# Kernel tuning notes

Measured on AMD Instinct MI355X. Metric: run time of the kernel, lower is better.

Reference implementation:

```python
import jax, jax.numpy as jnp
import numpy as np

B, H, S, D = 4, 8, 2048, 64

def setup_inputs() -> dict:
    key = jax.random.key(0)
    k1, k2 = jax.random.split(key)
    q = jax.random.normal(k1, (B, H, S, D), dtype=jnp.float32)
    kv = jax.random.normal(k2, (B, H, S, D), dtype=jnp.float32)
    mask = jnp.zeros((1, 1, S, S), dtype=jnp.float32)
    return {"q": q, "kv": kv, "mask": mask}

def reference(q, kv, mask):
    # score = q @ kv^T / sqrt(d_k) + mask ; softmax over last dim ; @ kv
    d_k = jnp.asarray(kv.shape[-1], dtype=q.dtype)
    score = jnp.einsum('bhqd,bhkd->bhqk', q, kv) / jnp.sqrt(d_k)
    score = score + mask
    attn = jax.nn.softmax(score, axis=-1)
    out = jnp.einsum('bhqk,bhkd->bhqd', attn, kv)
    return out
```

## Files before the change

kernel.cpp:

```cpp
#include <hip/hip_runtime.h>
#include <hip/hip_bf16.h>
#include <stdint.h>


typedef __bf16 bf16;
typedef __attribute__((ext_vector_type(8))) __bf16 bf16x8;
typedef __attribute__((ext_vector_type(4))) __bf16 bf16x4;
typedef __attribute__((ext_vector_type(4))) float floatx4;

#define SLEN 2048
#define DH   64
#define BR   64
#define BC   64
#define NKT  (SLEN / BC)
#define NEP  (NKT / 2)
#define NQT  (SLEN / BR)
#define BH_N 32
#define LOG2E 1.44269504088896341f

#define CHB_L  1024
#define IMGB_L 8192
#define IMGE_G 4096
#define BUF2   (4 * IMGB_L)

#define AS1 __attribute__((address_space(1)))
#define AS3 __attribute__((address_space(3)))

static __device__ inline void gload_lds16(const void* g, void* l) {
    __builtin_amdgcn_global_load_lds((const AS1 uint32_t*)g, (AS3 uint32_t*)l, 16, 0, 0);
}

static __device__ inline float fexp2(float x) {
    return __builtin_amdgcn_exp2f(x);
}

static_assert(BH_N == NQT, "prep kernel folds bh and qt onto one grid axis");

static __device__ inline int phys_key(int l) {
    int h = l >> 5, l5 = l & 31, q = l5 >> 3, j = l5 & 7;
    return 32 * h + (j < 4 ? 4 * q + j : 16 + 4 * q + (j - 4));
}

__global__ __launch_bounds__(256) void kv_prep(
    const float* __restrict__ kv, const float* __restrict__ mask,
    bf16* __restrict__ kvK, bf16* __restrict__ kvT, int* __restrict__ flags)
{
    __shared__ bf16 Tl[64 * 72];
    __shared__ int wany[4];
    const int kt = blockIdx.x, z = blockIdx.y;
    const int t = threadIdx.x;

    float acc = 0.f;
#pragma unroll
    for (int i = 0; i < 4; ++i) {
        int f = i * 256 + t;
        int row = f >> 4, c4 = (f & 15) * 4;
        const float4 v = *(const float4*)(mask + (size_t)(z * BR + row) * SLEN + kt * BC + c4);
        acc = fmaxf(acc, fmaxf(fmaxf(fabsf(v.x), fabsf(v.y)), fmaxf(fabsf(v.z), fabsf(v.w))));
    }
    unsigned long long any = __ballot(acc != 0.f);
    if ((t & 63) == 0) wany[t >> 6] = (any != 0ull) ? 1 : 0;

    const float* src = kv + ((size_t)z * SLEN + kt * BC) * DH;
#pragma unroll
    for (int i = 0; i < 4; ++i) {
        int f = i * 256 + t;
        int key = f >> 4, d4 = (f & 15) * 4;
        float4 v = *(const float4*)(src + (size_t)key * DH + d4);
        bf16x4 b; b[0] = (bf16)v.x; b[1] = (bf16)v.y; b[2] = (bf16)v.z; b[3] = (bf16)v.w;
        *(bf16x4*)&Tl[key * 72 + d4] = b;
    }
    __syncthreads();
    if (t == 0) flags[z * NKT + kt] = wany[0] | wany[1] | wany[2] | wany[3];

    bf16* outK = kvK + ((size_t)z * NKT + kt) * IMGE_G;
#pragma unroll
    for (int i = 0; i < 2; ++i) {
        int G = i * 256 + t;
        int c = G >> 6, L = G & 63, rl = L >> 3, p = L & 7;
        int g = (p - rl - 4 * (c & 1)) & 7, key = 8 * c + rl;
        bf16x8 w = *(const bf16x8*)&Tl[key * 72 + g * 8];
        *(bf16x8*)(outK + (size_t)G * 8) = w;
    }
    bf16* outV = kvT + ((size_t)z * NKT + kt) * IMGE_G;
#pragma unroll
    for (int i = 0; i < 2; ++i) {
        int G = i * 256 + t;
        int c = G >> 6, L = G & 63, dl = L >> 3, p = L & 7;
        int g = (p - dl - 4 * (c & 1)) & 7, d = 8 * c + dl;
        bf16x8 w;
#pragma unroll
        for (int j = 0; j < 8; ++j)
            w[j] = Tl[phys_key(8 * g + j) * 72 + d];
        *(bf16x8*)(outV + (size_t)G * 8) = w;
    }
}

__global__ __launch_bounds__(512) void attn_fwd13(
    const float* __restrict__ q, const float* __restrict__ mask,
    const int* __restrict__ flags,
    const bf16* __restrict__ kvK, const bf16* __restrict__ kvT,
    float* __restrict__ out)
{
    __shared__ __align__(16) char smem[2 * BUF2];

    const int bh = blockIdx.x;
    const int qt = blockIdx.y;
    const int q0 = qt * 128;
    const int t = threadIdx.x;
    const int wave = t >> 6, lane = t & 63;
    const int ln16 = lane & 15, quad = lane >> 4;
    const int ln8 = ln16 & 7, hb = ln16 >> 3;

    const float qscale = 0.125f * LOG2E;
    bf16x8 aq[2];
    {
        const float* qrow = q + ((size_t)bh * SLEN + q0 + wave * 16 + ln16) * DH;
#pragma unroll
        for (int kc = 0; kc < 2; ++kc) {
            float4 f0 = *(const float4*)(qrow + kc * 32 + quad * 8);
            float4 f1 = *(const float4*)(qrow + kc * 32 + quad * 8 + 4);
            bf16x8 a;
            a[0] = (bf16)(f0.x * qscale); a[1] = (bf16)(f0.y * qscale);
            a[2] = (bf16)(f0.z * qscale); a[3] = (bf16)(f0.w * qscale);
            a[4] = (bf16)(f1.x * qscale); a[5] = (bf16)(f1.y * qscale);
            a[6] = (bf16)(f1.z * qscale); a[7] = (bf16)(f1.w * qscale);
            aq[kc] = a;
        }
    }

    const int fqt = qt * 2 + (wave >> 2);
    unsigned fmask;
    {
        int ld = (lane < 32) ? flags[fqt * NKT + lane] : 0;
        fmask = (unsigned)__ballot(ld != 0);
    }

    const int kbase0 = hb * CHB_L + ln8 * 128 + (((quad + ln8 + 4 * hb) & 7) << 4);
    const int kbase1 = hb * CHB_L + ln8 * 128 + (((quad + 4 + ln8 + 4 * hb) & 7) << 4);

    floatx4 o[4];
#pragma unroll
    for (int dt = 0; dt < 4; ++dt) o[dt] = (floatx4){0.f, 0.f, 0.f, 0.f};
    float m_run = -3.0e38f, l_run = 0.f;

    const bf16* kvKb = kvK + (size_t)bh * NKT * IMGE_G;
    const bf16* kvTb = kvT + (size_t)bh * NKT * IMGE_G;

    {
        char* B0 = smem;
        gload_lds16(kvKb + (size_t)wave * 512 + lane * 8,           B0 +             wave * CHB_L);
        gload_lds16(kvTb + (size_t)wave * 512 + lane * 8,           B0 + IMGB_L +    wave * CHB_L);
        gload_lds16(kvKb + IMGE_G + (size_t)wave * 512 + lane * 8,  B0 + 2*IMGB_L +  wave * CHB_L);
        gload_lds16(kvTb + IMGE_G + (size_t)wave * 512 + lane * 8,  B0 + 3*IMGB_L +  wave * CHB_L);
    }

    for (int e = 0; e < NEP; ++e) {
        __syncthreads();

        if (e + 1 < NEP) {
            char* Bn = smem + ((e + 1) & 1) * BUF2;
            const bf16* gK0 = kvKb + (size_t)(2 * e + 2) * IMGE_G;
            const bf16* gV0 = kvTb + (size_t)(2 * e + 2) * IMGE_G;
            gload_lds16(gK0 + (size_t)wave * 512 + lane * 8,          Bn +            wave * CHB_L);
            gload_lds16(gV0 + (size_t)wave * 512 + lane * 8,          Bn + IMGB_L +   wave * CHB_L);
            gload_lds16(gK0 + IMGE_G + (size_t)wave * 512 + lane * 8, Bn + 2*IMGB_L + wave * CHB_L);
            gload_lds16(gV0 + IMGE_G + (size_t)wave * 512 + lane * 8, Bn + 3*IMGB_L + wave * CHB_L);
        }

        const char* B  = smem + (e & 1) * BUF2;
        const char* K0 = B;
        const char* V0 = B + IMGB_L;
        const char* K1 = B + 2 * IMGB_L;
        const char* V1 = B + 3 * IMGB_L;

        floatx4 s0[4], s1[4];
#pragma unroll
        for (int nt = 0; nt < 4; ++nt) {
            bf16x8 a0 = *(const bf16x8*)(K0 + nt * 2048 + kbase0);
            bf16x8 a1 = *(const bf16x8*)(K0 + nt * 2048 + kbase1);
            floatx4 acc = (floatx4){0.f, 0.f, 0.f, 0.f};
            acc = __builtin_amdgcn_mfma_f32_16x16x32_bf16(a0, aq[0], acc, 0, 0, 0);
            acc = __builtin_amdgcn_mfma_f32_16x16x32_bf16(a1, aq[1], acc, 0, 0, 0);
            s0[nt] = acc;
        }
#pragma unroll
        for (int nt = 0; nt < 4; ++nt) {
            bf16x8 a0 = *(const bf16x8*)(K1 + nt * 2048 + kbase0);
            bf16x8 a1 = *(const bf16x8*)(K1 + nt * 2048 + kbase1);
            floatx4 acc = (floatx4){0.f, 0.f, 0.f, 0.f};
            acc = __builtin_amdgcn_mfma_f32_16x16x32_bf16(a0, aq[0], acc, 0, 0, 0);
            acc = __builtin_amdgcn_mfma_f32_16x16x32_bf16(a1, aq[1], acc, 0, 0, 0);
            s1[nt] = acc;
        }

        if (fmask & (1u << (2 * e))) {
            const float* mrow = mask + (size_t)(q0 + wave * 16 + ln16) * SLEN + (2 * e) * BC;
#pragma unroll
            for (int nt = 0; nt < 4; ++nt) {
                float4 mv = *(const float4*)(mrow + 16 * nt + quad * 4);
                s0[nt][0] += mv.x * LOG2E; s0[nt][1] += mv.y * LOG2E;
                s0[nt][2] += mv.z * LOG2E; s0[nt][3] += mv.w * LOG2E;
            }
        }
        if (fmask & (1u << (2 * e + 1))) {
            const float* mrow = mask + (size_t)(q0 + wave * 16 + ln16) * SLEN + (2 * e + 1) * BC;
#pragma unroll
            for (int nt = 0; nt < 4; ++nt) {
                float4 mv = *(const float4*)(mrow + 16 * nt + quad * 4);
                s1[nt][0] += mv.x * LOG2E; s1[nt][1] += mv.y * LOG2E;
                s1[nt][2] += mv.z * LOG2E; s1[nt][3] += mv.w * LOG2E;
            }
        }

        float tm0 = s0[0][0], tm1 = s1[0][0];
#pragma unroll
        for (int nt = 0; nt < 4; ++nt)
#pragma unroll
            for (int r = 0; r < 4; ++r) {
                tm0 = fmaxf(tm0, s0[nt][r]);
                tm1 = fmaxf(tm1, s1[nt][r]);
            }
        float tmax = fmaxf(tm0, tm1);
        tmax = fmaxf(tmax, __shfl_xor(tmax, 16));
        tmax = fmaxf(tmax, __shfl_xor(tmax, 32));
        float mnew = fmaxf(m_run, tmax);
        unsigned long long grew = __ballot(mnew > m_run);
        float alpha = fexp2(m_run - mnew);
        m_run = mnew;

        float rs = 0.f;
        bf16x8 pf00, pf01, pf10, pf11;
#pragma unroll
        for (int r = 0; r < 4; ++r) {
            float a0 = fexp2(s0[0][r] - mnew);
            float a1 = fexp2(s0[1][r] - mnew);
            float a2 = fexp2(s0[2][r] - mnew);
            float a3 = fexp2(s0[3][r] - mnew);
            float b0 = fexp2(s1[0][r] - mnew);
            float b1 = fexp2(s1[1][r] - mnew);
            float b2 = fexp2(s1[2][r] - mnew);
            float b3 = fexp2(s1[3][r] - mnew);
            rs += ((a0 + a1) + (a2 + a3)) + ((b0 + b1) + (b2 + b3));
            pf00[r] = (bf16)a0; pf00[4 + r] = (bf16)a1;
            pf01[r] = (bf16)a2; pf01[4 + r] = (bf16)a3;
            pf10[r] = (bf16)b0; pf10[4 + r] = (bf16)b1;
            pf11[r] = (bf16)b2; pf11[4 + r] = (bf16)b3;
        }
        rs += __shfl_xor(rs, 16);
        rs += __shfl_xor(rs, 32);

        if (grew) {
            l_run = l_run * alpha + rs;
            float a0 = __shfl(alpha, quad * 4 + 0);
            float a1 = __shfl(alpha, quad * 4 + 1);
            float a2 = __shfl(alpha, quad * 4 + 2);
            float a3 = __shfl(alpha, quad * 4 + 3);
#pragma unroll
            for (int dt = 0; dt < 4; ++dt) {
                o[dt][0] *= a0; o[dt][1] *= a1; o[dt][2] *= a2; o[dt][3] *= a3;
            }
        } else {
            l_run += rs;
        }

#pragma unroll
        for (int dt = 0; dt < 4; ++dt) {
            bf16x8 v0 = *(const bf16x8*)(V0 + dt * 2048 + kbase0);
            bf16x8 v1 = *(const bf16x8*)(V0 + dt * 2048 + kbase1);
            o[dt] = __builtin_amdgcn_mfma_f32_16x16x32_bf16(pf00, v0, o[dt], 0, 0, 0);
            o[dt] = __builtin_amdgcn_mfma_f32_16x16x32_bf16(pf01, v1, o[dt], 0, 0, 0);
        }
#pragma unroll
        for (int dt = 0; dt < 4; ++dt) {
            bf16x8 v0 = *(const bf16x8*)(V1 + dt * 2048 + kbase0);
            bf16x8 v1 = *(const bf16x8*)(V1 + dt * 2048 + kbase1);
            o[dt] = __builtin_amdgcn_mfma_f32_16x16x32_bf16(pf10, v0, o[dt], 0, 0, 0);
            o[dt] = __builtin_amdgcn_mfma_f32_16x16x32_bf16(pf11, v1, o[dt], 0, 0, 0);
        }
    }

    float l0 = __shfl(l_run, quad * 4 + 0);
    float l1 = __shfl(l_run, quad * 4 + 1);
    float l2 = __shfl(l_run, quad * 4 + 2);
    float l3 = __shfl(l_run, quad * 4 + 3);
    float i0 = 1.f / l0, i1 = 1.f / l1, i2 = 1.f / l2, i3 = 1.f / l3;
    float* ob = out + ((size_t)bh * SLEN + q0 + wave * 16) * DH;
#pragma unroll
    for (int dt = 0; dt < 4; ++dt) {
        int col = ln16 + 16 * dt;
        ob[(quad * 4 + 0) * DH + col] = o[dt][0] * i0;
        ob[(quad * 4 + 1) * DH + col] = o[dt][1] * i1;
        ob[(quad * 4 + 2) * DH + col] = o[dt][2] * i2;
        ob[(quad * 4 + 3) * DH + col] = o[dt][3] * i3;
    }
}

#define LDT 72
__global__ __launch_bounds__(256) void attn_mask_flags(
    const float* __restrict__ mask, int* __restrict__ flags)
{
    const int kt = blockIdx.x, qt = blockIdx.y;
    const int t = threadIdx.x;
    float acc = 0.f;
#pragma unroll
    for (int i = 0; i < 4; ++i) {
        int f = i * 256 + t;
        int row = f >> 4, c4 = (f & 15) * 4;
        const float4 v = *(const float4*)(mask + (size_t)(qt * BR + row) * SLEN + kt * BC + c4);
        acc = fmaxf(acc, fmaxf(fmaxf(fabsf(v.x), fabsf(v.y)), fmaxf(fabsf(v.z), fabsf(v.w))));
    }
    unsigned long long any = __ballot(acc != 0.f);
    __shared__ int wany[4];
    if ((t & 63) == 0) wany[t >> 6] = (any != 0ull) ? 1 : 0;
    __syncthreads();
    if (t == 0) flags[qt * NKT + kt] = wany[0] | wany[1] | wany[2] | wany[3];
}

__global__ __launch_bounds__(256) void attn_fwd(
    const float* __restrict__ q, const float* __restrict__ kv,
    const float* __restrict__ mask, const int* __restrict__ flags,
    float* __restrict__ out)
{
    __shared__ __align__(16) bf16 Kl[BC * LDT];
    __shared__ __align__(16) bf16 Vt[DH * LDT];
    __shared__ __align__(16) bf16 Pl[BR * LDT];

    const int qt = blockIdx.x;
    const int bh = blockIdx.y;
    const int q0 = qt * BR;
    const int t = threadIdx.x;
    const int wave = t >> 6, lane = t & 63;
    const int ln16 = lane & 15, quad = lane >> 4;

    const float qscale = 0.125f * LOG2E;
    bf16x8 aq[2];
    {
        const float* qrow = q + ((size_t)bh * SLEN + q0 + wave * 16 + ln16) * DH;
#pragma unroll
        for (int kc = 0; kc < 2; ++kc) {
            float4 f0 = *(const float4*)(qrow + kc * 32 + quad * 8);
            float4 f1 = *(const float4*)(qrow + kc * 32 + quad * 8 + 4);
            bf16x8 a;
            a[0] = (bf16)(f0.x * qscale); a[1] = (bf16)(f0.y * qscale);
            a[2] = (bf16)(f0.z * qscale); a[3] = (bf16)(f0.w * qscale);
            a[4] = (bf16)(f1.x * qscale); a[5] = (bf16)(f1.y * qscale);
            a[6] = (bf16)(f1.z * qscale); a[7] = (bf16)(f1.w * qscale);
            aq[kc] = a;
        }
    }

    floatx4 o[4];
#pragma unroll
    for (int dt = 0; dt < 4; ++dt) o[dt] = (floatx4){0.f, 0.f, 0.f, 0.f};
    float m_run[4], l_run[4];
#pragma unroll
    for (int r = 0; r < 4; ++r) { m_run[r] = -3.0e38f; l_run[r] = 0.f; }

    const float* kvb = kv + (size_t)bh * SLEN * DH;

    for (int kt = 0; kt < NKT; ++kt) {
        float4 st[4];
        const float* kvt = kvb + (size_t)kt * BC * DH;
#pragma unroll
        for (int i = 0; i < 4; ++i) {
            int f = i * 256 + t;
            st[i] = *(const float4*)(kvt + (size_t)f * 4);
        }
        __syncthreads();
#pragma unroll
        for (int i = 0; i < 4; ++i) {
            int f = i * 256 + t;
            int key = f >> 4, d4 = (f & 15) * 4;
            bf16 b0 = (bf16)st[i].x, b1 = (bf16)st[i].y, b2 = (bf16)st[i].z, b3 = (bf16)st[i].w;
            *(bf16x4*)&Kl[key * LDT + d4] = (bf16x4){b0, b1, b2, b3};
            Vt[(d4 + 0) * LDT + key] = b0;
            Vt[(d4 + 1) * LDT + key] = b1;
            Vt[(d4 + 2) * LDT + key] = b2;
            Vt[(d4 + 3) * LDT + key] = b3;
        }
        __syncthreads();

        floatx4 s[4];
#pragma unroll
        for (int nt = 0; nt < 4; ++nt) {
            s[nt] = (floatx4){0.f, 0.f, 0.f, 0.f};
#pragma unroll
            for (int kc = 0; kc < 2; ++kc) {
                bf16x8 bk = *(const bf16x8*)&Kl[(ln16 + 16 * nt) * LDT + kc * 32 + quad * 8];
                s[nt] = __builtin_amdgcn_mfma_f32_16x16x32_bf16(aq[kc], bk, s[nt], 0, 0, 0);
            }
        }

        if (!flags || flags[qt * NKT + kt]) {
            const float* mrow = mask + (size_t)(q0 + quad * 4) * SLEN + kt * BC + ln16;
#pragma unroll
            for (int r = 0; r < 4; ++r)
#pragma unroll
                for (int nt = 0; nt < 4; ++nt)
                    s[nt][r] += mrow[(size_t)r * SLEN + nt * 16] * LOG2E;
        }

#pragma unroll
        for (int r = 0; r < 4; ++r) {
            float mx = fmaxf(fmaxf(s[0][r], s[1][r]), fmaxf(s[2][r], s[3][r]));
            mx = fmaxf(mx, __shfl_xor(mx, 1));
            mx = fmaxf(mx, __shfl_xor(mx, 2));
            mx = fmaxf(mx, __shfl_xor(mx, 4));
            mx = fmaxf(mx, __shfl_xor(mx, 8));
            float mnew = fmaxf(m_run[r], mx);
            float alpha = exp2f(m_run[r] - mnew);
            m_run[r] = mnew;
            float rs = 0.f;
#pragma unroll
            for (int nt = 0; nt < 4; ++nt) {
                float p = exp2f(s[nt][r] - mnew);
                s[nt][r] = p;
                rs += p;
            }
            rs += __shfl_xor(rs, 1);
            rs += __shfl_xor(rs, 2);
            rs += __shfl_xor(rs, 4);
            rs += __shfl_xor(rs, 8);
            l_run[r] = l_run[r] * alpha + rs;
#pragma unroll
            for (int dt = 0; dt < 4; ++dt) o[dt][r] *= alpha;
        }

#pragma unroll
        for (int nt = 0; nt < 4; ++nt)
#pragma unroll
            for (int r = 0; r < 4; ++r)
                Pl[(wave * 16 + quad * 4 + r) * LDT + ln16 + 16 * nt] = (bf16)s[nt][r];

#pragma unroll
        for (int kc2 = 0; kc2 < 2; ++kc2) {
            bf16x8 pfr = *(const bf16x8*)&Pl[(wave * 16 + ln16) * LDT + kc2 * 32 + quad * 8];
#pragma unroll
            for (int dt = 0; dt < 4; ++dt) {
                bf16x8 vfr = *(const bf16x8*)&Vt[(ln16 + 16 * dt) * LDT + kc2 * 32 + quad * 8];
                o[dt] = __builtin_amdgcn_mfma_f32_16x16x32_bf16(pfr, vfr, o[dt], 0, 0, 0);
            }
        }
    }

#pragma unroll
    for (int r = 0; r < 4; ++r) {
        float inv = 1.0f / l_run[r];
        int qrow = q0 + wave * 16 + quad * 4 + r;
        float* orow = out + ((size_t)bh * SLEN + qrow) * DH;
#pragma unroll
        for (int dt = 0; dt < 4; ++dt)
            orow[ln16 + 16 * dt] = o[dt][r] * inv;
    }
}

extern "C" void kernel_launch(void* const* d_in, const int* in_sizes, int n_in,
                              void* d_out, int out_size, void* d_ws, size_t ws_size,
                              hipStream_t stream)
{
    const float* q    = (const float*)d_in[0];
    const float* kv   = (const float*)d_in[1];
    const float* mask = (const float*)d_in[2];
    float* out = (float*)d_out;

    const size_t kvKoff = 4096;
    const size_t kvToff = kvKoff + (size_t)BH_N * NKT * IMGE_G * 2;
    const size_t need   = kvToff + (size_t)BH_N * NKT * IMGE_G * 2;

    if (ws_size >= need) {
        int*  flags = (int*)d_ws;
        bf16* kvK   = (bf16*)((char*)d_ws + kvKoff);
        bf16* kvT   = (bf16*)((char*)d_ws + kvToff);
        kv_prep<<<dim3(NKT, BH_N), 256, 0, stream>>>(kv, mask, kvK, kvT, flags);
        attn_fwd13<<<dim3(BH_N, SLEN / 128), 512, 0, stream>>>(q, mask, flags, kvK, kvT, out);
    } else {
        int* flags = nullptr;
        if (ws_size >= (size_t)NQT * NKT * sizeof(int)) {
            flags = (int*)d_ws;
            attn_mask_flags<<<dim3(NKT, NQT), 256, 0, stream>>>(mask, flags);
        }
        attn_fwd<<<dim3(NQT, BH_N), 256, 0, stream>>>(q, kv, mask, flags, out);
    }
}
```

Before: 140.7 us.

## Switch attention to 32x32x16 MFMA tiles with 4 waves per block

Rewrites the main attention kernel to use 32x32x16 bf16 MFMA instead of 16x16x32. Each of 4 waves now owns 32 query rows instead of 16, and the block shrinks from 512 to 256 threads with 2 blocks per CU. The P operand is rearranged in registers with permlane32_swap instead of relying on a permuted key order, so the V prep drops the phys_key remap. Row-max and row-sum reductions need only one cross-half shuffle, and output stores become float4. The aim is fewer MFMA issues and less LDS operand traffic per FLOP, at the cost of more accumulator registers and possible occupancy pressure.

```diff
diff --git a/kernel.cpp b/kernel.cpp
--- a/kernel.cpp
+++ b/kernel.cpp
@@ -7,6 +7,9 @@
 typedef __attribute__((ext_vector_type(8))) __bf16 bf16x8;
 typedef __attribute__((ext_vector_type(4))) __bf16 bf16x4;
 typedef __attribute__((ext_vector_type(4))) float floatx4;
+typedef __attribute__((ext_vector_type(16))) float floatx16;
+typedef __attribute__((ext_vector_type(4))) int int4v;
+typedef __attribute__((ext_vector_type(2))) unsigned int uint2v;
 
 #define SLEN 2048
 #define DH   64
@@ -36,11 +39,6 @@
 
 static_assert(BH_N == NQT, "prep kernel folds bh and qt onto one grid axis");
 
-static __device__ inline int phys_key(int l) {
-    int h = l >> 5, l5 = l & 31, q = l5 >> 3, j = l5 & 7;
-    return 32 * h + (j < 4 ? 4 * q + j : 16 + 4 * q + (j - 4));
-}
-
 __global__ __launch_bounds__(256) void kv_prep(
     const float* __restrict__ kv, const float* __restrict__ mask,
     bf16* __restrict__ kvK, bf16* __restrict__ kvT, int* __restrict__ flags)
@@ -91,12 +89,12 @@
         bf16x8 w;
 #pragma unroll
         for (int j = 0; j < 8; ++j)
-            w[j] = Tl[phys_key(8 * g + j) * 72 + d];
+            w[j] = Tl[(8 * g + j) * 72 + d];
         *(bf16x8*)(outV + (size_t)G * 8) = w;
     }
 }
 
-__global__ __launch_bounds__(512) void attn_fwd13(
+__global__ __launch_bounds__(256, 2) void attn_fwd14(
     const float* __restrict__ q, const float* __restrict__ mask,
     const int* __restrict__ flags,
     const bf16* __restrict__ kvK, const bf16* __restrict__ kvT,
@@ -108,192 +106,183 @@
     const int qt = blockIdx.y;
     const int q0 = qt * 128;
     const int t = threadIdx.x;
-    const int wave = t >> 6, lane = t & 63;
-    const int ln16 = lane & 15, quad = lane >> 4;
-    const int ln8 = ln16 & 7, hb = ln16 >> 3;
+    const int w = t >> 6, lane = t & 63;
+    const int r5 = lane & 31, h = lane >> 5;
+    const int c3 = r5 >> 3, rl = lane & 7;
 
     const float qscale = 0.125f * LOG2E;
-    bf16x8 aq[2];
+    bf16x8 qf[4];
     {
-        const float* qrow = q + ((size_t)bh * SLEN + q0 + wave * 16 + ln16) * DH;
-#pragma unroll
-        for (int kc = 0; kc < 2; ++kc) {
-            float4 f0 = *(const float4*)(qrow + kc * 32 + quad * 8);
-            float4 f1 = *(const float4*)(qrow + kc * 32 + quad * 8 + 4);
+        const float* qrow = q + ((size_t)bh * SLEN + q0 + w * 32 + r5) * DH;
+#pragma unroll
+        for (int s = 0; s < 4; ++s) {
+            float4 f0 = *(const float4*)(qrow + 16 * s + 8 * h);
+            float4 f1 = *(const float4*)(qrow + 16 * s + 8 * h + 4);
             bf16x8 a;
             a[0] = (bf16)(f0.x * qscale); a[1] = (bf16)(f0.y * qscale);
             a[2] = (bf16)(f0.z * qscale); a[3] = (bf16)(f0.w * qscale);
             a[4] = (bf16)(f1.x * qscale); a[5] = (bf16)(f1.y * qscale);
             a[6] = (bf16)(f1.z * qscale); a[7] = (bf16)(f1.w * qscale);
-            aq[kc] = a;
-        }
-    }
-
-    const int fqt = qt * 2 + (wave >> 2);
+            qf[s] = a;
+        }
+    }
+
+    const int fqt = qt * 2 + (w >> 1);
     unsigned fmask;
     {
         int ld = (lane < 32) ? flags[fqt * NKT + lane] : 0;
         fmask = (unsigned)__ballot(ld != 0);
     }
 
-    const int kbase0 = hb * CHB_L + ln8 * 128 + (((quad + ln8 + 4 * hb) & 7) << 4);
-    const int kbase1 = hb * CHB_L + ln8 * 128 + (((quad + 4 + ln8 + 4 * hb) & 7) << 4);
-
-    floatx4 o[4];
-#pragma unroll
-    for (int dt = 0; dt < 4; ++dt) o[dt] = (floatx4){0.f, 0.f, 0.f, 0.f};
+    int addr4[4];
+#pragma unroll
+    for (int s = 0; s < 4; ++s) {
+        int slot = (2 * s + h + rl + 4 * (c3 & 1)) & 7;
+        addr4[s] = c3 * 1024 + rl * 128 + slot * 16;
+    }
+
+    floatx16 o[2];
+#pragma unroll
+    for (int dt = 0; dt < 2; ++dt)
+#pragma unroll
+        for (int i = 0; i < 16; ++i) o[dt][i] = 0.f;
     float m_run = -3.0e38f, l_run = 0.f;
 
     const bf16* kvKb = kvK + (size_t)bh * NKT * IMGE_G;
     const bf16* kvTb = kvT + (size_t)bh * NKT * IMGE_G;
 
-    {
-        char* B0 = smem;
-        gload_lds16(kvKb + (size_t)wave * 512 + lane * 8,           B0 +             wave * CHB_L);
-        gload_lds16(kvTb + (size_t)wave * 512 + lane * 8,           B0 + IMGB_L +    wave * CHB_L);
-        gload_lds16(kvKb + IMGE_G + (size_t)wave * 512 + lane * 8,  B0 + 2*IMGB_L +  wave * CHB_L);
-        gload_lds16(kvTb + IMGE_G + (size_t)wave * 512 + lane * 8,  B0 + 3*IMGB_L +  wave * CHB_L);
-    }
+    auto stage = [&](int t2, char* Bn) {
+        const bf16* gK = kvKb + (size_t)t2 * IMGE_G;
+        const bf16* gV = kvTb + (size_t)t2 * IMGE_G;
+#pragma unroll
+        for (int cc = 0; cc < 2; ++cc) {
+            const int c = 2 * w + cc;
+            gload_lds16(gK + (size_t)c * 512 + lane * 8,          Bn +              c * CHB_L);
+            gload_lds16(gV + (size_t)c * 512 + lane * 8,          Bn + IMGB_L +     c * CHB_L);
+            gload_lds16(gK + IMGE_G + (size_t)c * 512 + lane * 8, Bn + 2 * IMGB_L + c * CHB_L);
+            gload_lds16(gV + IMGE_G + (size_t)c * 512 + lane * 8, Bn + 3 * IMGB_L + c * CHB_L);
+        }
+    };
+
+    stage(0, smem);
 
     for (int e = 0; e < NEP; ++e) {
         __syncthreads();
 
-        if (e + 1 < NEP) {
-            char* Bn = smem + ((e + 1) & 1) * BUF2;
-            const bf16* gK0 = kvKb + (size_t)(2 * e + 2) * IMGE_G;
-            const bf16* gV0 = kvTb + (size_t)(2 * e + 2) * IMGE_G;
-            gload_lds16(gK0 + (size_t)wave * 512 + lane * 8,          Bn +            wave * CHB_L);
-            gload_lds16(gV0 + (size_t)wave * 512 + lane * 8,          Bn + IMGB_L +   wave * CHB_L);
-            gload_lds16(gK0 + IMGE_G + (size_t)wave * 512 + lane * 8, Bn + 2*IMGB_L + wave * CHB_L);
-            gload_lds16(gV0 + IMGE_G + (size_t)wave * 512 + lane * 8, Bn + 3*IMGB_L + wave * CHB_L);
-        }
-
-        const char* B  = smem + (e & 1) * BUF2;
-        const char* K0 = B;
-        const char* V0 = B + IMGB_L;
-        const char* K1 = B + 2 * IMGB_L;
-        const char* V1 = B + 3 * IMGB_L;
-
-        floatx4 s0[4], s1[4];
-#pragma unroll
-        for (int nt = 0; nt < 4; ++nt) {
-            bf16x8 a0 = *(const bf16x8*)(K0 + nt * 2048 + kbase0);
-            bf16x8 a1 = *(const bf16x8*)(K0 + nt * 2048 + kbase1);
-            floatx4 acc = (floatx4){0.f, 0.f, 0.f, 0.f};
-            acc = __builtin_amdgcn_mfma_f32_16x16x32_bf16(a0, aq[0], acc, 0, 0, 0);
-            acc = __builtin_amdgcn_mfma_f32_16x16x32_bf16(a1, aq[1], acc, 0, 0, 0);
-            s0[nt] = acc;
-        }
-#pragma unroll
-        for (int nt = 0; nt < 4; ++nt) {
-            bf16x8 a0 = *(const bf16x8*)(K1 + nt * 2048 + kbase0);
-            bf16x8 a1 = *(const bf16x8*)(K1 + nt * 2048 + kbase1);
-            floatx4 acc = (floatx4){0.f, 0.f, 0.f, 0.f};
-            acc = __builtin_amdgcn_mfma_f32_16x16x32_bf16(a0, aq[0], acc, 0, 0, 0);
-            acc = __builtin_amdgcn_mfma_f32_16x16x32_bf16(a1, aq[1], acc, 0, 0, 0);
-            s1[nt] = acc;
-        }
-
-        if (fmask & (1u << (2 * e))) {
-            const float* mrow = mask + (size_t)(q0 + wave * 16 + ln16) * SLEN + (2 * e) * BC;
-#pragma unroll
-            for (int nt = 0; nt < 4; ++nt) {
-                float4 mv = *(const float4*)(mrow + 16 * nt + quad * 4);
-                s0[nt][0] += mv.x * LOG2E; s0[nt][1] += mv.y * LOG2E;
-                s0[nt][2] += mv.z * LOG2E; s0[nt][3] += mv.w * LOG2E;
-            }
-        }
-        if (fmask & (1u << (2 * e + 1))) {
-            const float* mrow = mask + (size_t)(q0 + wave * 16 + ln16) * SLEN + (2 * e + 1) * BC;
-#pragma unroll
-            for (int nt = 0; nt < 4; ++nt) {
-                float4 mv = *(const float4*)(mrow + 16 * nt + quad * 4);
-                s1[nt][0] += mv.x * LOG2E; s1[nt][1] += mv.y * LOG2E;
-                s1[nt][2] += mv.z * LOG2E; s1[nt][3] += mv.w * LOG2E;
-            }
-        }
-
-        float tm0 = s0[0][0], tm1 = s1[0][0];
-#pragma unroll
-        for (int nt = 0; nt < 4; ++nt)
-#pragma unroll
-            for (int r = 0; r < 4; ++r) {
-                tm0 = fmaxf(tm0, s0[nt][r]);
-                tm1 = fmaxf(tm1, s1[nt][r]);
-            }
-        float tmax = fmaxf(tm0, tm1);
-        tmax = fmaxf(tmax, __shfl_xor(tmax, 16));
+        if (e + 1 < NEP) stage(2 * e + 2, smem + ((e + 1) & 1) * BUF2);
+
+        const char* B = smem + (e & 1) * BUF2;
+
+        floatx16 s[4];
+#pragma unroll
+        for (int T = 0; T < 4; ++T) {
+            const char* Kimg = B + (T >> 1) * (2 * IMGB_L) + (T & 1) * 4096;
+            floatx16 acc;
+#pragma unroll
+            for (int i = 0; i < 16; ++i) acc[i] = 0.f;
+#pragma unroll
+            for (int ss = 0; ss < 4; ++ss) {
+                bf16x8 kf = *(const bf16x8*)(Kimg + addr4[ss]);
+                acc = __builtin_amdgcn_mfma_f32_32x32x16_bf16(kf, qf[ss], acc, 0, 0, 0);
+            }
+            s[T] = acc;
+        }
+
+#pragma unroll
+        for (int T = 0; T < 4; ++T) {
+            if (fmask & (1u << (2 * e + (T >> 1)))) {
+                const float* mrow = mask + (size_t)(q0 + w * 32 + r5) * SLEN
+                                    + e * 128 + T * 32 + 4 * h;
+#pragma unroll
+                for (int g4 = 0; g4 < 4; ++g4) {
+                    float4 mv = *(const float4*)(mrow + 8 * g4);
+                    s[T][4 * g4 + 0] += mv.x * LOG2E;
+                    s[T][4 * g4 + 1] += mv.y * LOG2E;
+                    s[T][4 * g4 + 2] += mv.z * LOG2E;
+                    s[T][4 * g4 + 3] += mv.w * LOG2E;
+                }
+            }
+        }
+
+        float tm[4];
+#pragma unroll
+        for (int T = 0; T < 4; ++T) {
+            float a0 = fmaxf(s[T][0], s[T][1]),   a1 = fmaxf(s[T][2], s[T][3]);
+            float a2 = fmaxf(s[T][4], s[T][5]),   a3 = fmaxf(s[T][6], s[T][7]);
+            float a4 = fmaxf(s[T][8], s[T][9]),   a5 = fmaxf(s[T][10], s[T][11]);
+            float a6 = fmaxf(s[T][12], s[T][13]), a7 = fmaxf(s[T][14], s[T][15]);
+            a0 = fmaxf(a0, a1); a2 = fmaxf(a2, a3); a4 = fmaxf(a4, a5); a6 = fmaxf(a6, a7);
+            tm[T] = fmaxf(fmaxf(a0, a2), fmaxf(a4, a6));
+        }
+        float tmax = fmaxf(fmaxf(tm[0], tm[1]), fmaxf(tm[2], tm[3]));
         tmax = fmaxf(tmax, __shfl_xor(tmax, 32));
         float mnew = fmaxf(m_run, tmax);
         unsigned long long grew = __ballot(mnew > m_run);
         float alpha = fexp2(m_run - mnew);
         m_run = mnew;
+        if (grew) {
+#pragma unroll
+            for (int dt = 0; dt < 2; ++dt)
+#pragma unroll
+                for (int i = 0; i < 16; ++i) o[dt][i] *= alpha;
+        }
 
         float rs = 0.f;
-        bf16x8 pf00, pf01, pf10, pf11;
-#pragma unroll
-        for (int r = 0; r < 4; ++r) {
-            float a0 = fexp2(s0[0][r] - mnew);
-            float a1 = fexp2(s0[1][r] - mnew);
-            float a2 = fexp2(s0[2][r] - mnew);
-            float a3 = fexp2(s0[3][r] - mnew);
-            float b0 = fexp2(s1[0][r] - mnew);
-            float b1 = fexp2(s1[1][r] - mnew);
-            float b2 = fexp2(s1[2][r] - mnew);
-            float b3 = fexp2(s1[3][r] - mnew);
-            rs += ((a0 + a1) + (a2 + a3)) + ((b0 + b1) + (b2 + b3));
-            pf00[r] = (bf16)a0; pf00[4 + r] = (bf16)a1;
-            pf01[r] = (bf16)a2; pf01[4 + r] = (bf16)a3;
-            pf10[r] = (bf16)b0; pf10[4 + r] = (bf16)b1;
-            pf11[r] = (bf16)b2; pf11[4 + r] = (bf16)b3;
-        }
-        rs += __shfl_xor(rs, 16);
+#pragma unroll
+        for (int T = 0; T < 4; ++T) {
+            float ev[16];
+#pragma unroll
+            for (int i = 0; i < 16; ++i) ev[i] = fexp2(s[T][i] - mnew);
+            float r0 = (ev[0] + ev[1]) + (ev[2] + ev[3]);
+            float r1 = (ev[4] + ev[5]) + (ev[6] + ev[7]);
+            float r2 = (ev[8] + ev[9]) + (ev[10] + ev[11]);
+            float r3 = (ev[12] + ev[13]) + (ev[14] + ev[15]);
+            rs += (r0 + r1) + (r2 + r3);
+
+            bf16x4 lA = { (bf16)ev[0],  (bf16)ev[1],  (bf16)ev[2],  (bf16)ev[3]  };
+            bf16x4 hA = { (bf16)ev[4],  (bf16)ev[5],  (bf16)ev[6],  (bf16)ev[7]  };
+            bf16x4 lB = { (bf16)ev[8],  (bf16)ev[9],  (bf16)ev[10], (bf16)ev[11] };
+            bf16x4 hB = { (bf16)ev[12], (bf16)ev[13], (bf16)ev[14], (bf16)ev[15] };
+            uint2v xA = __builtin_bit_cast(uint2v, lA);
+            uint2v yA = __builtin_bit_cast(uint2v, hA);
+            uint2v xB = __builtin_bit_cast(uint2v, lB);
+            uint2v yB = __builtin_bit_cast(uint2v, hB);
+            uint2v sA0 = __builtin_amdgcn_permlane32_swap(xA[0], yA[0], false, false);
+            uint2v sA1 = __builtin_amdgcn_permlane32_swap(xA[1], yA[1], false, false);
+            uint2v sB0 = __builtin_amdgcn_permlane32_swap(xB[0], yB[0], false, false);
+            uint2v sB1 = __builtin_amdgcn_permlane32_swap(xB[1], yB[1], false, false);
+            int4v pAi = { (int)sA0[0], (int)sA1[0], (int)sA0[1], (int)sA1[1] };
+            int4v pBi = { (int)sB0[0], (int)sB1[0], (int)sB0[1], (int)sB1[1] };
+            bf16x8 pfA = __builtin_bit_cast(bf16x8, pAi);
+            bf16x8 pfB = __builtin_bit_cast(bf16x8, pBi);
+
+            const char* Vimg = B + IMGB_L + (T >> 1) * (2 * IMGB_L);
+            const int uA = 2 * (T & 1), uB = uA + 1;
+#pragma unroll
+            for (int dt = 0; dt < 2; ++dt) {
+                bf16x8 vA = *(const bf16x8*)(Vimg + dt * 4096 + addr4[uA]);
+                o[dt] = __builtin_amdgcn_mfma_f32_32x32x16_bf16(vA, pfA, o[dt], 0, 0, 0);
+                bf16x8 vB = *(const bf16x8*)(Vimg + dt * 4096 + addr4[uB]);
+                o[dt] = __builtin_amdgcn_mfma_f32_32x32x16_bf16(vB, pfB, o[dt], 0, 0, 0);
+            }
+        }
         rs += __shfl_xor(rs, 32);
-
-        if (grew) {
-            l_run = l_run * alpha + rs;
-            float a0 = __shfl(alpha, quad * 4 + 0);
-            float a1 = __shfl(alpha, quad * 4 + 1);
-            float a2 = __shfl(alpha, quad * 4 + 2);
-            float a3 = __shfl(alpha, quad * 4 + 3);
-#pragma unroll
-            for (int dt = 0; dt < 4; ++dt) {
-                o[dt][0] *= a0; o[dt][1] *= a1; o[dt][2] *= a2; o[dt][3] *= a3;
-            }
-        } else {
-            l_run += rs;
-        }
-
-#pragma unroll
-        for (int dt = 0; dt < 4; ++dt) {
-            bf16x8 v0 = *(const bf16x8*)(V0 + dt * 2048 + kbase0);
-            bf16x8 v1 = *(const bf16x8*)(V0 + dt * 2048 + kbase1);
-            o[dt] = __builtin_amdgcn_mfma_f32_16x16x32_bf16(pf00, v0, o[dt], 0, 0, 0);
-            o[dt] = __builtin_amdgcn_mfma_f32_16x16x32_bf16(pf01, v1, o[dt], 0, 0, 0);
-        }
-#pragma unroll
-        for (int dt = 0; dt < 4; ++dt) {
-            bf16x8 v0 = *(const bf16x8*)(V1 + dt * 2048 + kbase0);
-            bf16x8 v1 = *(const bf16x8*)(V1 + dt * 2048 + kbase1);
-            o[dt] = __builtin_amdgcn_mfma_f32_16x16x32_bf16(pf10, v0, o[dt], 0, 0, 0);
-            o[dt] = __builtin_amdgcn_mfma_f32_16x16x32_bf16(pf11, v1, o[dt], 0, 0, 0);
-        }
-    }
-
-    float l0 = __shfl(l_run, quad * 4 + 0);
-    float l1 = __shfl(l_run, quad * 4 + 1);
-    float l2 = __shfl(l_run, quad * 4 + 2);
-    float l3 = __shfl(l_run, quad * 4 + 3);
-    float i0 = 1.f / l0, i1 = 1.f / l1, i2 = 1.f / l2, i3 = 1.f / l3;
-    float* ob = out + ((size_t)bh * SLEN + q0 + wave * 16) * DH;
-#pragma unroll
-    for (int dt = 0; dt < 4; ++dt) {
-        int col = ln16 + 16 * dt;
-        ob[(quad * 4 + 0) * DH + col] = o[dt][0] * i0;
-        ob[(quad * 4 + 1) * DH + col] = o[dt][1] * i1;
-        ob[(quad * 4 + 2) * DH + col] = o[dt][2] * i2;
-        ob[(quad * 4 + 3) * DH + col] = o[dt][3] * i3;
-    }
+        l_run = (grew ? l_run * alpha : l_run) + rs;
+    }
+
+    const float inv = 1.0f / l_run;
+    float* ob = out + ((size_t)bh * SLEN + q0 + w * 32 + r5) * DH + 4 * h;
+#pragma unroll
+    for (int dt = 0; dt < 2; ++dt)
+#pragma unroll
+        for (int k = 0; k < 4; ++k) {
+            float4 v;
+            v.x = o[dt][4 * k + 0] * inv;
+            v.y = o[dt][4 * k + 1] * inv;
+            v.z = o[dt][4 * k + 2] * inv;
+            v.w = o[dt][4 * k + 3] * inv;
+            *(float4*)(ob + dt * 32 + 8 * k) = v;
+        }
 }
 
 #define LDT 72
@@ -473,7 +462,7 @@
         bf16* kvK   = (bf16*)((char*)d_ws + kvKoff);
         bf16* kvT   = (bf16*)((char*)d_ws + kvToff);
         kv_prep<<<dim3(NKT, BH_N), 256, 0, stream>>>(kv, mask, kvK, kvT, flags);
-        attn_fwd13<<<dim3(BH_N, SLEN / 128), 512, 0, stream>>>(q, mask, flags, kvK, kvT, out);
+        attn_fwd14<<<dim3(BH_N, SLEN / 128), 256, 0, stream>>>(q, mask, flags, kvK, kvT, out);
     } else {
         int* flags = nullptr;
         if (ws_size >= (size_t)NQT * NKT * sizeof(int)) {
```

After: 141.6 us. No clear change (+0.7%).
